# Kernel optimization log

Measured on AMD Instinct MI355X. Metric: run time of the kernel, lower is better.

## Reference

```python
import jax, jax.numpy as jnp
import numpy as np

M = 8192
N = 8192

def setup_inputs() -> dict:
    key = jax.random.key(0)
    d_noised = jax.random.normal(key, (M, N), dtype=jnp.float32)
    threshold = jnp.float32(0.5)
    return {"d_noised": d_noised, "threshold": threshold}

def reference(d_noised, threshold):
    # Intended semantics of the original Python loops:
    # for each pixel (i, j), look at the 4 diagonal neighbors
    # (dx != 0 and dy != 0 -> dx, dy in {-1, +1}), and if the absolute
    # depth difference to any in-bounds diagonal neighbor is <= threshold,
    # mark the pixel as connected. The original stores into
    # adjacency_matrix[j][i], i.e. the transposed (n, m) layout.
    m, n = d_noised.shape
    # Pad with a huge value so out-of-bounds neighbors always fail the
    # |diff| <= threshold test (equivalent to the bounds checks).
    big = jnp.asarray(jnp.finfo(d_noised.dtype).max, d_noised.dtype)
    padded = jnp.pad(d_noised, 1, constant_values=big)  # [m+2, n+2]
    connected = jnp.zeros((m, n), dtype=bool)
    for dy in (-1, 1):
        for dx in (-1, 1):
            nb = padded[1 + dy:1 + dy + m, 1 + dx:1 + dx + n]  # shifted view
            connected = connected | (jnp.abs(nb - d_noised) <= threshold)
    # adjacency_matrix[j, i] = connected[i, j]
    return connected.T
```

## Files before the change

### kernel.cpp

```cpp
#include <hip/hip_runtime.h>
#include <float.h>


typedef int iv4 __attribute__((ext_vector_type(4)));

__device__ __forceinline__ void load_row(const float* __restrict__ d, int y, int x0, int xl,
                                         float* r, float& eL, float& eR) {
    if ((unsigned)y < 8192u) {
        const float4 a = *reinterpret_cast<const float4*>(d + ((size_t)y << 13) + xl);
        const float4 b = *reinterpret_cast<const float4*>(d + ((size_t)y << 13) + xl + 4);
        r[0] = a.x; r[1] = a.y; r[2] = a.z; r[3] = a.w;
        r[4] = b.x; r[5] = b.y; r[6] = b.z; r[7] = b.w;
        eL = (x0 > 0)          ? d[((size_t)y << 13) + x0 - 1]   : FLT_MAX;
        eR = (x0 + 512 < 8192) ? d[((size_t)y << 13) + x0 + 512] : FLT_MAX;
    } else {
#pragma unroll
        for (int i = 0; i < 8; ++i) r[i] = FLT_MAX;
        eL = eR = FLT_MAX;
    }
}

__global__ __launch_bounds__(256, 4)
void pass1_kernel(const float* __restrict__ d, const float* __restrict__ thrp,
                  unsigned char* __restrict__ bm) {
    const float thr = thrp[0];
    const int tid  = threadIdx.x;
    const int lane = tid & 63;
    const int wid  = blockIdx.x * 4 + (tid >> 6);
    const int strip = wid & 15;
    const int band  = wid >> 4;
    const int x0 = strip * 512;
    const int yb = band * 32;
    const int xl = x0 + 8 * lane;

    float rA[8], rB[8], rC[8], rD[8];
    float eA, eB, eC, eD, fA, fB, fC, fD;

    load_row(d, yb - 1, x0, xl, rA, eA, fA);
    load_row(d, yb,     x0, xl, rB, eB, fB);
    load_row(d, yb + 1, x0, xl, rC, eC, fC);

    for (int y = yb; y < yb + 32; ++y) {
        const int yn = y + 2;
        if (yn <= yb + 32) load_row(d, yn, x0, xl, rD, eD, fD);

        float lA = __shfl_up(rA[7], 1);   if (lane == 0)  lA = eA;
        float hA = __shfl_down(rA[0], 1); if (lane == 63) hA = fA;
        float lC = __shfl_up(rC[7], 1);   if (lane == 0)  lC = eC;
        float hC = __shfl_down(rC[0], 1); if (lane == 63) hC = fC;

        unsigned byte = 0;
#pragma unroll
        for (int k = 0; k < 8; ++k) {
            const float c  = rB[k];
            const float tl = (k == 0) ? lA : rA[k - 1];
            const float tr = (k == 7) ? hA : rA[k + 1];
            const float bl = (k == 0) ? lC : rC[k - 1];
            const float br = (k == 7) ? hC : rC[k + 1];
            const bool conn = (fabsf(tl - c) <= thr) | (fabsf(tr - c) <= thr) |
                              (fabsf(bl - c) <= thr) | (fabsf(br - c) <= thr);
            byte |= (conn ? 1u : 0u) << k;
        }
        bm[(size_t)y * 1024 + (x0 >> 3) + lane] = (unsigned char)byte;

#pragma unroll
        for (int i = 0; i < 8; ++i) { rA[i] = rB[i]; rB[i] = rC[i]; rC[i] = rD[i]; }
        eA = eB; eB = eC; eC = eD;
        fA = fB; fB = fC; fC = fD;
    }
}

__global__ __launch_bounds__(256, 8)
void pass2_kernel(const unsigned* __restrict__ bm32, int* __restrict__ out) {
    const int tid  = threadIdx.x;
    const int lane = tid & 63;
    const int wid  = blockIdx.x * 4 + (tid >> 6);
    const int xt = wid >> 3;
    const int yw = wid & 7;
    const int x0 = xt * 8;
    const int y0 = yw * 1024;
    const int xw = xt >> 2;
    const int b0 = (xt & 3) * 8;

    unsigned w[4][4];
#pragma unroll
    for (int c = 0; c < 4; ++c)
#pragma unroll
        for (int j = 0; j < 4; ++j)
            w[c][j] = bm32[(size_t)(y0 + c * 256 + 4 * lane + j) * 256 + xw];

#pragma unroll
    for (int r = 0; r < 8; ++r) {
        const int bit = b0 + r;
        int* rowp = out + ((size_t)(x0 + r) << 13) + y0 + 4 * lane;
#pragma unroll
        for (int c = 0; c < 4; ++c) {
            iv4 o;
            o.x = (int)((w[c][0] >> bit) & 1u);
            o.y = (int)((w[c][1] >> bit) & 1u);
            o.z = (int)((w[c][2] >> bit) & 1u);
            o.w = (int)((w[c][3] >> bit) & 1u);
            __builtin_nontemporal_store(o, reinterpret_cast<iv4*>(rowp + c * 256));
        }
    }
}

#define BIG4 make_float4(FLT_MAX, FLT_MAX, FLT_MAX, FLT_MAX)

template<bool EDGE>
__device__ __forceinline__ void recon_body(const float* __restrict__ d, float thr,
                                           int* __restrict__ out, int bx, int by, int tid) {
    const int xq = tid & 15;
    const int yq = tid >> 4;
    const int gx = bx * 64 + 4 * xq;
    const int gy = by * 64 + 4 * yq;
    float s[6][6];
#pragma unroll
    for (int j = 0; j < 6; ++j) {
        const int yy = gy - 1 + j;
        float4 a, b, c;
        if (!EDGE) {
            const float4* p = (const float4*)(d + ((size_t)yy << 13) + gx);
            a = p[-1]; b = p[0]; c = p[1];
        } else {
            const bool yok = (unsigned)yy < 8192u;
            const float4* p = (const float4*)(d + ((size_t)(yok ? yy : 0) << 13) + gx);
            a = (yok && gx >= 4)       ? p[-1] : BIG4;
            b = yok                    ? p[0]  : BIG4;
            c = (yok && gx + 7 < 8192) ? p[1]  : BIG4;
        }
        s[j][0] = a.w; s[j][1] = b.x; s[j][2] = b.y;
        s[j][3] = b.z; s[j][4] = b.w; s[j][5] = c.x;
    }
#pragma unroll
    for (int i = 0; i < 4; ++i) {
        int r[4];
#pragma unroll
        for (int k = 0; k < 4; ++k) {
            const float ctr = s[k + 1][i + 1];
            const bool conn = (fabsf(s[k][i]     - ctr) <= thr) |
                              (fabsf(s[k][i + 2] - ctr) <= thr) |
                              (fabsf(s[k + 2][i]     - ctr) <= thr) |
                              (fabsf(s[k + 2][i + 2] - ctr) <= thr);
            r[k] = conn ? 1 : 0;
        }
        *reinterpret_cast<int4*>(out + ((size_t)(gx + i) << 13) + gy) =
            make_int4(r[0], r[1], r[2], r[3]);
    }
}

__global__ __launch_bounds__(256, 4)
void recon_fallback(const float* __restrict__ d, const float* __restrict__ thrp,
                    int* __restrict__ out) {
    const float thr = thrp[0];
    const int bx = blockIdx.x, by = blockIdx.y;
    if (bx >= 1 && bx <= 126 && by >= 1 && by <= 126)
        recon_body<false>(d, thr, out, bx, by, threadIdx.x);
    else
        recon_body<true>(d, thr, out, bx, by, threadIdx.x);
}

extern "C" void kernel_launch(void* const* d_in, const int* in_sizes, int n_in,
                              void* d_out, int out_size, void* d_ws, size_t ws_size,
                              hipStream_t stream) {
    const float* d   = (const float*)d_in[0];
    const float* thr = (const float*)d_in[1];
    int* out = (int*)d_out;
    const size_t BM_BYTES = (size_t)8192 * 1024;

    if (ws_size >= BM_BYTES) {
        unsigned char* bm = (unsigned char*)d_ws;
        pass1_kernel<<<1024, 256, 0, stream>>>(d, thr, bm);
        pass2_kernel<<<2048, 256, 0, stream>>>((const unsigned*)bm, out);
    } else {
        recon_fallback<<<dim3(128, 128), 256, 0, stream>>>(d, thr, out);
    }
}
```

Baseline: 101.9 us.

## Transpose intermediate bitmap layout so both passes use contiguous vector accesses

Pass1 now keeps the 32 row-bytes of each lane's 8-column group in registers. At the end it writes them as two 16-byte nontemporal stores into a column-major bitmap, replacing one byte store per row. Pass2 reads one contiguous 16-byte vector per lane and redistributes the words through LDS within the wave. This replaces 16 strided 4-byte gathers per lane. The aim is fewer, better-coalesced memory transactions on the intermediate bitmap, at the cost of strided 32-byte writes in pass1 and an LDS round trip in pass2.

```diff
diff --git a/kernel.cpp b/kernel.cpp
--- a/kernel.cpp
+++ b/kernel.cpp
@@ -2,7 +2,8 @@
 #include <float.h>
 
 
-typedef int iv4 __attribute__((ext_vector_type(4)));
+typedef int  iv4 __attribute__((ext_vector_type(4)));
+typedef unsigned uv4 __attribute__((ext_vector_type(4)));
 
 __device__ __forceinline__ void load_row(const float* __restrict__ d, int y, int x0, int xl,
                                          float* r, float& eL, float& eR) {
@@ -40,6 +41,8 @@
     load_row(d, yb,     x0, xl, rB, eB, fB);
     load_row(d, yb + 1, x0, xl, rC, eC, fC);
 
+    unsigned w[8] = {0, 0, 0, 0, 0, 0, 0, 0};
+
     for (int y = yb; y < yb + 32; ++y) {
         const int yn = y + 2;
         if (yn <= yb + 32) load_row(d, yn, x0, xl, rD, eD, fD);
@@ -61,45 +64,58 @@
                               (fabsf(bl - c) <= thr) | (fabsf(br - c) <= thr);
             byte |= (conn ? 1u : 0u) << k;
         }
-        bm[(size_t)y * 1024 + (x0 >> 3) + lane] = (unsigned char)byte;
+        const int i = y - yb;
+        w[i >> 2] |= byte << (8 * (i & 3));
 
 #pragma unroll
-        for (int i = 0; i < 8; ++i) { rA[i] = rB[i]; rB[i] = rC[i]; rC[i] = rD[i]; }
+        for (int q = 0; q < 8; ++q) { rA[q] = rB[q]; rB[q] = rC[q]; rC[q] = rD[q]; }
         eA = eB; eB = eC; eC = eD;
         fA = fB; fB = fC; fC = fD;
     }
+
+    const int col = (x0 >> 3) + lane;
+    unsigned char* p = bm + (size_t)col * 8192 + yb;
+    uv4 lo; lo.x = w[0]; lo.y = w[1]; lo.z = w[2]; lo.w = w[3];
+    uv4 hi; hi.x = w[4]; hi.y = w[5]; hi.z = w[6]; hi.w = w[7];
+    __builtin_nontemporal_store(lo, reinterpret_cast<uv4*>(p));
+    __builtin_nontemporal_store(hi, reinterpret_cast<uv4*>(p + 16));
 }
 
 __global__ __launch_bounds__(256, 8)
-void pass2_kernel(const unsigned* __restrict__ bm32, int* __restrict__ out) {
+void pass2_kernel(const unsigned char* __restrict__ bm, int* __restrict__ out) {
+    __shared__ unsigned lds[4][256];
+
     const int tid  = threadIdx.x;
     const int lane = tid & 63;
-    const int wid  = blockIdx.x * 4 + (tid >> 6);
-    const int xt = wid >> 3;
-    const int yw = wid & 7;
-    const int x0 = xt * 8;
+    const int wv   = tid >> 6;
+    const int wid  = blockIdx.x * 4 + wv;
+    const int xcol = wid >> 3;
+    const int yw   = wid & 7;
+    const int x0 = xcol * 8;
     const int y0 = yw * 1024;
-    const int xw = xt >> 2;
-    const int b0 = (xt & 3) * 8;
 
-    unsigned w[4][4];
+    const uv4 bv = *reinterpret_cast<const uv4*>(bm + (size_t)xcol * 8192 + y0 + 16 * lane);
+    lds[wv][4 * lane + 0] = bv.x;
+    lds[wv][4 * lane + 1] = bv.y;
+    lds[wv][4 * lane + 2] = bv.z;
+    lds[wv][4 * lane + 3] = bv.w;
+    __builtin_amdgcn_s_waitcnt(0);
+
+    unsigned w[4];
 #pragma unroll
     for (int c = 0; c < 4; ++c)
-#pragma unroll
-        for (int j = 0; j < 4; ++j)
-            w[c][j] = bm32[(size_t)(y0 + c * 256 + 4 * lane + j) * 256 + xw];
+        w[c] = lds[wv][c * 64 + lane];
 
 #pragma unroll
     for (int r = 0; r < 8; ++r) {
-        const int bit = b0 + r;
         int* rowp = out + ((size_t)(x0 + r) << 13) + y0 + 4 * lane;
 #pragma unroll
         for (int c = 0; c < 4; ++c) {
             iv4 o;
-            o.x = (int)((w[c][0] >> bit) & 1u);
-            o.y = (int)((w[c][1] >> bit) & 1u);
-            o.z = (int)((w[c][2] >> bit) & 1u);
-            o.w = (int)((w[c][3] >> bit) & 1u);
+            o.x = (int)((w[c] >> (r))      & 1u);
+            o.y = (int)((w[c] >> (r + 8))  & 1u);
+            o.z = (int)((w[c] >> (r + 16)) & 1u);
+            o.w = (int)((w[c] >> (r + 24)) & 1u);
             __builtin_nontemporal_store(o, reinterpret_cast<iv4*>(rowp + c * 256));
         }
     }
@@ -171,7 +187,7 @@
     if (ws_size >= BM_BYTES) {
         unsigned char* bm = (unsigned char*)d_ws;
         pass1_kernel<<<1024, 256, 0, stream>>>(d, thr, bm);
-        pass2_kernel<<<2048, 256, 0, stream>>>((const unsigned*)bm, out);
+        pass2_kernel<<<2048, 256, 0, stream>>>(bm, out);
     } else {
         recon_fallback<<<dim3(128, 128), 256, 0, stream>>>(d, thr, out);
     }
```

New measurement: 100.6 us, median of 2. Within noise of the previous version (-1.3%).
